# Performance work log

Hardware: AMD Instinct MI355X
Metric: run time of the kernel (lower is better)

Reference implementation:

```python
import jax, jax.numpy as jnp
import numpy as np


def setup_inputs() -> dict:
    key = jax.random.key(0)
    ks = jax.random.split(key, 8)
    B, E = 1024, 8
    dims = [480, 512, 512, 311]
    inp = {
        "x": jax.random.normal(ks[0], (B, dims[0]), dtype=jnp.float32),
        "weight_blend": jax.random.uniform(ks[1], (E, B), dtype=jnp.float32),
        "w0": jax.random.normal(ks[2], (E, dims[1], dims[0]), dtype=jnp.float32) * 0.05,
        "b0": jax.random.normal(ks[3], (E, dims[1]), dtype=jnp.float32) * 0.05,
        "w1": jax.random.normal(ks[4], (E, dims[2], dims[1]), dtype=jnp.float32) * 0.05,
        "b1": jax.random.normal(ks[5], (E, dims[2]), dtype=jnp.float32) * 0.05,
        "w2": jax.random.normal(ks[6], (E, dims[3], dims[2]), dtype=jnp.float32) * 0.05,
        "b2": jax.random.normal(ks[7], (E, dims[3]), dtype=jnp.float32) * 0.05,
    }
    return inp


def _blend_layer(h, blend, w, b):
    # Original: W_b = sum_e blend[e,b] * w[e]  (materializes [B, d_out, d_in]),
    # then matmul(W_b, h) + bias_b. Fused einsum computes identical math.
    out = jnp.einsum("eb,eoi,bi->bo", blend, w, h)
    out = out + jnp.einsum("eb,eo->bo", blend, b)
    return out


def reference(x, weight_blend, w0, b0, w1, b1, w2, b2):
    # dropout layers are identity (training=False / keep_prob=1)
    h = _blend_layer(x, weight_blend, w0, b0)
    h = jax.nn.elu(h)
    h = _blend_layer(h, weight_blend, w1, b1)
    h = jax.nn.elu(h)
    h = _blend_layer(h, weight_blend, w2, b2)  # no activation on final layer
    return h
```

## Files before the change

### kernel.cpp

```cpp
#include <hip/hip_runtime.h>

typedef __attribute__((ext_vector_type(8))) short short8;
typedef __attribute__((ext_vector_type(4))) float f32x4;

__device__ __forceinline__ unsigned short f2bf(float f) {
    unsigned u = __builtin_bit_cast(unsigned, f);
    unsigned r = (u + 0x7FFFu + ((u >> 16) & 1u)) >> 16;
    return (unsigned short)r;
}
__device__ __forceinline__ float bf2f(unsigned short u) {
    unsigned v = ((unsigned)u) << 16;
    return __builtin_bit_cast(float, v);
}

__device__ __forceinline__ void gload16(const unsigned short* g, unsigned short* l) {
    __builtin_amdgcn_global_load_lds(
        (const __attribute__((address_space(1))) void*)g,
        (__attribute__((address_space(3))) void*)l,
        16, 0, 0);
}

#define WAITV(N) asm volatile("s_waitcnt vmcnt(" #N ")" ::: "memory")
#define WAITL0() asm volatile("s_waitcnt lgkmcnt(0)" ::: "memory")
#define BAR() do { asm volatile("" ::: "memory"); __builtin_amdgcn_s_barrier(); asm volatile("" ::: "memory"); } while (0)

__device__ __forceinline__ short8 lds_read_swz(const unsigned short* tile, int row, int colb) {
    int off = row * 64 + colb;
    off ^= ((off >> 7) & 7) << 4;
    return *(const short8*)((const char*)tile + off);
}

__device__ __forceinline__ void cvt_chunk(const float* __restrict__ src,
                                          unsigned short* __restrict__ dst, int t) {
    const float4* s4 = (const float4*)src;
    float4 a = s4[2 * t], b = s4[2 * t + 1];
    union { unsigned short u[8]; int4 v; } r;
    r.u[0] = f2bf(a.x); r.u[1] = f2bf(a.y); r.u[2] = f2bf(a.z); r.u[3] = f2bf(a.w);
    r.u[4] = f2bf(b.x); r.u[5] = f2bf(b.y); r.u[6] = f2bf(b.z); r.u[7] = f2bf(b.w);
    ((int4*)dst)[t] = r.v;
}

__device__ __forceinline__ short8 pack8(float4 a, float4 b) {
    short8 p;
    p[0] = (short)f2bf(a.x); p[1] = (short)f2bf(a.y);
    p[2] = (short)f2bf(a.z); p[3] = (short)f2bf(a.w);
    p[4] = (short)f2bf(b.x); p[5] = (short)f2bf(b.y);
    p[6] = (short)f2bf(b.z); p[7] = (short)f2bf(b.w);
    return p;
}

__global__ __launch_bounds__(512) void k_gemm0(
    const float* __restrict__ A, const float* __restrict__ W,
    const float* __restrict__ blend, const float* __restrict__ bias,
    unsigned short* __restrict__ Y,
    const float* __restrict__ csrc, unsigned short* __restrict__ cdst)
{
    __shared__ unsigned short As[2][4096];
    __shared__ unsigned short Bs[2][4096];

    const int e  = blockIdx.z;
    const int bm = blockIdx.y * 128;
    const int on = blockIdx.x * 128;
    const int t  = threadIdx.x, lane = t & 63, w = t >> 6;
    const int wr = w >> 2, wc = w & 3;

    const int sr = lane >> 2, sce = (lane & 3) * 8;
    const int ra = w * 16 + sr;
    const float* gA = A + (size_t)(bm + ra) * 480 + sce;
    const float* gB = W + ((size_t)e * 512 + (on + ra)) * 480 + sce;

    int woff = ra * 64 + (lane & 3) * 16;
    woff ^= ((woff >> 7) & 7) << 4;

    float4 La0[3], La1[3], Lb0[3], Lb1[3];
    #pragma unroll
    for (int s = 0; s < 3; ++s) {
        int k0 = s * 32;
        La0[s] = *(const float4*)(gA + k0); La1[s] = *(const float4*)(gA + k0 + 4);
        Lb0[s] = *(const float4*)(gB + k0); Lb1[s] = *(const float4*)(gB + k0 + 4);
    }

    f32x4 acc[4][2] = {};

    #pragma unroll
    for (int kt = 0; kt < 15; ++kt) {
        const int s = kt % 3, buf = kt & 1;
        *(short8*)((char*)As[buf] + woff) = pack8(La0[s], La1[s]);
        *(short8*)((char*)Bs[buf] + woff) = pack8(Lb0[s], Lb1[s]);
        WAITL0();
        BAR();
        if (kt + 3 < 15) {
            int k0 = (kt + 3) * 32;
            La0[s] = *(const float4*)(gA + k0); La1[s] = *(const float4*)(gA + k0 + 4);
            Lb0[s] = *(const float4*)(gB + k0); Lb1[s] = *(const float4*)(gB + k0 + 4);
        }
        short8 af[4], bfr[2];
        #pragma unroll
        for (int fm = 0; fm < 4; ++fm)
            af[fm] = lds_read_swz(As[buf], wr * 64 + fm * 16 + (lane & 15), (lane >> 4) * 16);
        #pragma unroll
        for (int fn = 0; fn < 2; ++fn)
            bfr[fn] = lds_read_swz(Bs[buf], wc * 32 + fn * 16 + (lane & 15), (lane >> 4) * 16);
        #pragma unroll
        for (int fm = 0; fm < 4; ++fm)
            #pragma unroll
            for (int fn = 0; fn < 2; ++fn)
                acc[fm][fn] = __builtin_amdgcn_mfma_f32_16x16x32_bf16(
                    af[fm], bfr[fn], acc[fm][fn], 0, 0, 0);
    }

    const float* blendE = blend + e * 1024;
    const float* biasE  = bias + (size_t)e * 512;
    unsigned short* Ye  = Y + (size_t)e * 1024 * 512;
    #pragma unroll
    for (int fm = 0; fm < 4; ++fm) {
        int i0 = bm + wr * 64 + fm * 16 + (lane >> 4) * 4;
        float4 bl = *(const float4*)&blendE[i0];
        #pragma unroll
        for (int fn = 0; fn < 2; ++fn) {
            int j = on + wc * 32 + fn * 16 + (lane & 15);
            float bs = biasE[j];
            #pragma unroll
            for (int r = 0; r < 4; ++r)
                Ye[(size_t)(i0 + r) * 512 + j] = f2bf((acc[fm][fn][r] + bs) * ((&bl.x)[r]));
        }
    }

    int lb = (blockIdx.z * 8 + blockIdx.y) * 4 + blockIdx.x;
    cvt_chunk(csrc, cdst, lb * 1024 + threadIdx.x);
    cvt_chunk(csrc, cdst, lb * 1024 + 512 + threadIdx.x);
}

__global__ __launch_bounds__(512) void k_gemm(
    const unsigned short* __restrict__ A,
    const unsigned short* __restrict__ W,
    const float* __restrict__ blend, const float* __restrict__ bias,
    unsigned short* __restrict__ Y,
    int N, int ldy,
    const float* __restrict__ csrc, unsigned short* __restrict__ cdst, int nchunk)
{
    __shared__ unsigned short As[4][4096];
    __shared__ unsigned short Bs[4][4096];

    const int e  = blockIdx.z;
    const int bm = blockIdx.y * 128;
    const int on = blockIdx.x * 128;
    const int t  = threadIdx.x, lane = t & 63, w = t >> 6;
    const int wr = w >> 2, wc = w & 3;

    const unsigned short* Wt = W + (size_t)e * N * 512;
    const int l2 = lane ^ ((lane >> 3) & 7);
    const int sr = l2 >> 2, sce = (l2 & 3) * 8;
    const int ra = w * 16 + sr;
    int rb = on + ra; if (rb > N - 1) rb = N - 1;
    const unsigned short* gA = A  + (size_t)(bm + ra) * 512 + sce;
    const unsigned short* gB = Wt + (size_t)rb * 512 + sce;

#define STAGE(buf, kt) do { int _k0 = (kt) * 32;                       \
        gload16(gA + _k0, &As[(buf)][w * 512]);                        \
        gload16(gB + _k0, &Bs[(buf)][w * 512]); } while (0)

#define COMPUTE(cur) do {                                                          \
        short8 af[4], bfr[2];                                                      \
        _Pragma("unroll")                                                          \
        for (int fm = 0; fm < 4; ++fm)                                             \
            af[fm] = lds_read_swz(As[(cur)], wr * 64 + fm * 16 + (lane & 15), (lane >> 4) * 16); \
        _Pragma("unroll")                                                          \
        for (int fn = 0; fn < 2; ++fn)                                             \
            bfr[fn] = lds_read_swz(Bs[(cur)], wc * 32 + fn * 16 + (lane & 15), (lane >> 4) * 16); \
        _Pragma("unroll")                                                          \
        for (int fm = 0; fm < 4; ++fm)                                             \
            _Pragma("unroll")                                                      \
            for (int fn = 0; fn < 2; ++fn)                                         \
                acc[fm][fn] = __builtin_amdgcn_mfma_f32_16x16x32_bf16(             \
                    af[fm], bfr[fn], acc[fm][fn], 0, 0, 0);                        \
    } while (0)

    f32x4 acc[4][2] = {};
    STAGE(0, 0); STAGE(1, 1); STAGE(2, 2);

    for (int kt = 0; kt < 13; ++kt) {
        WAITV(4);
        BAR();
        STAGE((kt + 3) & 3, kt + 3);
        COMPUTE(kt & 3);
    }
    WAITV(4); BAR(); COMPUTE(1);
    WAITV(2); BAR(); COMPUTE(2);
    WAITV(0); BAR(); COMPUTE(3);
#undef STAGE

    const float* blendE = blend + e * 1024;
    const float* biasE  = bias + (size_t)e * N;
    unsigned short* Ye  = Y + (size_t)e * 1024 * ldy;
    #pragma unroll
    for (int fm = 0; fm < 4; ++fm) {
        int i0 = bm + wr * 64 + fm * 16 + (lane >> 4) * 4;
        float4 bl = *(const float4*)&blendE[i0];
        #pragma unroll
        for (int fn = 0; fn < 2; ++fn) {
            int j = on + wc * 32 + fn * 16 + (lane & 15);
            if (j < N) {
                float bs = biasE[j];
                #pragma unroll
                for (int r = 0; r < 4; ++r)
                    Ye[(size_t)(i0 + r) * ldy + j] = f2bf((acc[fm][fn][r] + bs) * ((&bl.x)[r]));
            }
        }
    }

    if (cdst) {
        int lb = (blockIdx.z * 8 + blockIdx.y) * gridDim.x + blockIdx.x;
        #pragma unroll
        for (int q = 0; q < 2; ++q) {
            int tl = q * 512 + threadIdx.x;
            if (tl < nchunk) cvt_chunk(csrc, cdst, lb * nchunk + tl);
        }
    }
}

__global__ __launch_bounds__(256) void k_reduce8(
    const unsigned short* __restrict__ Y, unsigned short* __restrict__ out)
{
    int idx = blockIdx.x * 256 + threadIdx.x;
    int b  = idx >> 6;
    int o0 = (idx & 63) * 8;
    size_t base = (size_t)b * 512 + o0;
    float s[8] = {};
    #pragma unroll
    for (int p = 0; p < 8; ++p) {
        int4 v = *(const int4*)&Y[base + (size_t)p * 1024 * 512];
        const unsigned short* u = (const unsigned short*)&v;
        #pragma unroll
        for (int r = 0; r < 8; ++r) s[r] += bf2f(u[r]);
    }
    union { unsigned short u[8]; int4 v; } rr;
    #pragma unroll
    for (int r = 0; r < 8; ++r) {
        float v = (s[r] > 0.f) ? s[r] : expm1f(s[r]);
        rr.u[r] = f2bf(v);
    }
    *(int4*)&out[base] = rr.v;
}

__global__ __launch_bounds__(256) void k_reduce_last(
    const unsigned short* __restrict__ Y, float* __restrict__ out)
{
    int idx = blockIdx.x * 256 + threadIdx.x;
    if (idx >= 1024 * 40) return;
    int b  = idx / 40;
    int o0 = (idx - b * 40) * 8;
    size_t base = (size_t)b * 320 + o0;
    float s[8] = {};
    #pragma unroll
    for (int p = 0; p < 8; ++p) {
        int4 v = *(const int4*)&Y[base + (size_t)p * 1024 * 320];
        const unsigned short* u = (const unsigned short*)&v;
        #pragma unroll
        for (int r = 0; r < 8; ++r) s[r] += bf2f(u[r]);
    }
    #pragma unroll
    for (int r = 0; r < 8; ++r)
        if (o0 + r < 311) out[(size_t)b * 311 + o0 + r] = s[r];
}

extern "C" void kernel_launch(void* const* d_in, const int* in_sizes, int n_in,
                              void* d_out, int out_size, void* d_ws, size_t ws_size,
                              hipStream_t stream) {
    const float* x     = (const float*)d_in[0];
    const float* blend = (const float*)d_in[1];
    const float* w0    = (const float*)d_in[2];
    const float* b0    = (const float*)d_in[3];
    const float* w1    = (const float*)d_in[4];
    const float* b1    = (const float*)d_in[5];
    const float* w2    = (const float*)d_in[6];
    const float* b2    = (const float*)d_in[7];

    char* ws = (char*)d_ws;
    unsigned short* w1b = (unsigned short*)(ws + 0);
    unsigned short* w2b = (unsigned short*)(ws + 4194304);
    unsigned short* h1b = (unsigned short*)(ws + 6742016);
    unsigned short* h2b = (unsigned short*)(ws + 7790592);
    unsigned short* yb  = (unsigned short*)(ws + 8839168);

    k_gemm0<<<dim3(4, 8, 8), 512, 0, stream>>>(x, w0, blend, b0, yb, w1, w1b);
    k_reduce8<<<256, 256, 0, stream>>>(yb, h1b);

    k_gemm<<<dim3(4, 8, 8), 512, 0, stream>>>(h1b, w1b, blend, b1, yb, 512, 512,
                                              w2, w2b, 622);
    k_reduce8<<<256, 256, 0, stream>>>(yb, h2b);

    k_gemm<<<dim3(3, 8, 8), 512, 0, stream>>>(h2b, w2b, blend, b2, yb, 311, 320,
                                              nullptr, nullptr, 0);
    k_reduce_last<<<160, 256, 0, stream>>>(yb, (float*)d_out);
}
```

Before: 54.13 us.

## Fuse expert-sum reduction and ELU into the next GEMM's A-tile load

Removes the two standalone reduce kernels and has each subsequent GEMM read all 8 per-expert partial outputs, sum them, and apply ELU while building the bf16 A tile in LDS. This saves two launches and the write and re-read of the reduced activations. In exchange, every GEMM block re-reads the 8 expert slices for its rows, so each reduction is repeated across all N-tiles and experts, which multiplies global traffic for A by 8 and adds ALU work. The async global_load_lds 4-stage pipeline is replaced by a register-staged double buffer.

```diff
diff --git a/kernel.cpp b/kernel.cpp
--- a/kernel.cpp
+++ b/kernel.cpp
@@ -11,13 +11,6 @@
 __device__ __forceinline__ float bf2f(unsigned short u) {
     unsigned v = ((unsigned)u) << 16;
     return __builtin_bit_cast(float, v);
-}
-
-__device__ __forceinline__ void gload16(const unsigned short* g, unsigned short* l) {
-    __builtin_amdgcn_global_load_lds(
-        (const __attribute__((address_space(1))) void*)g,
-        (__attribute__((address_space(3))) void*)l,
-        16, 0, 0);
 }
 
 #define WAITV(N) asm volatile("s_waitcnt vmcnt(" #N ")" ::: "memory")
@@ -48,117 +41,6 @@
     p[6] = (short)f2bf(b.z); p[7] = (short)f2bf(b.w);
     return p;
 }
-
-__global__ __launch_bounds__(512) void k_gemm0(
-    const float* __restrict__ A, const float* __restrict__ W,
-    const float* __restrict__ blend, const float* __restrict__ bias,
-    unsigned short* __restrict__ Y,
-    const float* __restrict__ csrc, unsigned short* __restrict__ cdst)
-{
-    __shared__ unsigned short As[2][4096];
-    __shared__ unsigned short Bs[2][4096];
-
-    const int e  = blockIdx.z;
-    const int bm = blockIdx.y * 128;
-    const int on = blockIdx.x * 128;
-    const int t  = threadIdx.x, lane = t & 63, w = t >> 6;
-    const int wr = w >> 2, wc = w & 3;
-
-    const int sr = lane >> 2, sce = (lane & 3) * 8;
-    const int ra = w * 16 + sr;
-    const float* gA = A + (size_t)(bm + ra) * 480 + sce;
-    const float* gB = W + ((size_t)e * 512 + (on + ra)) * 480 + sce;
-
-    int woff = ra * 64 + (lane & 3) * 16;
-    woff ^= ((woff >> 7) & 7) << 4;
-
-    float4 La0[3], La1[3], Lb0[3], Lb1[3];
-    #pragma unroll
-    for (int s = 0; s < 3; ++s) {
-        int k0 = s * 32;
-        La0[s] = *(const float4*)(gA + k0); La1[s] = *(const float4*)(gA + k0 + 4);
-        Lb0[s] = *(const float4*)(gB + k0); Lb1[s] = *(const float4*)(gB + k0 + 4);
-    }
-
-    f32x4 acc[4][2] = {};
-
-    #pragma unroll
-    for (int kt = 0; kt < 15; ++kt) {
-        const int s = kt % 3, buf = kt & 1;
-        *(short8*)((char*)As[buf] + woff) = pack8(La0[s], La1[s]);
-        *(short8*)((char*)Bs[buf] + woff) = pack8(Lb0[s], Lb1[s]);
-        WAITL0();
-        BAR();
-        if (kt + 3 < 15) {
-            int k0 = (kt + 3) * 32;
-            La0[s] = *(const float4*)(gA + k0); La1[s] = *(const float4*)(gA + k0 + 4);
-            Lb0[s] = *(const float4*)(gB + k0); Lb1[s] = *(const float4*)(gB + k0 + 4);
-        }
-        short8 af[4], bfr[2];
-        #pragma unroll
-        for (int fm = 0; fm < 4; ++fm)
-            af[fm] = lds_read_swz(As[buf], wr * 64 + fm * 16 + (lane & 15), (lane >> 4) * 16);
-        #pragma unroll
-        for (int fn = 0; fn < 2; ++fn)
-            bfr[fn] = lds_read_swz(Bs[buf], wc * 32 + fn * 16 + (lane & 15), (lane >> 4) * 16);
-        #pragma unroll
-        for (int fm = 0; fm < 4; ++fm)
-            #pragma unroll
-            for (int fn = 0; fn < 2; ++fn)
-                acc[fm][fn] = __builtin_amdgcn_mfma_f32_16x16x32_bf16(
-                    af[fm], bfr[fn], acc[fm][fn], 0, 0, 0);
-    }
-
-    const float* blendE = blend + e * 1024;
-    const float* biasE  = bias + (size_t)e * 512;
-    unsigned short* Ye  = Y + (size_t)e * 1024 * 512;
-    #pragma unroll
-    for (int fm = 0; fm < 4; ++fm) {
-        int i0 = bm + wr * 64 + fm * 16 + (lane >> 4) * 4;
-        float4 bl = *(const float4*)&blendE[i0];
-        #pragma unroll
-        for (int fn = 0; fn < 2; ++fn) {
-            int j = on + wc * 32 + fn * 16 + (lane & 15);
-            float bs = biasE[j];
-            #pragma unroll
-            for (int r = 0; r < 4; ++r)
-                Ye[(size_t)(i0 + r) * 512 + j] = f2bf((acc[fm][fn][r] + bs) * ((&bl.x)[r]));
-        }
-    }
-
-    int lb = (blockIdx.z * 8 + blockIdx.y) * 4 + blockIdx.x;
-    cvt_chunk(csrc, cdst, lb * 1024 + threadIdx.x);
-    cvt_chunk(csrc, cdst, lb * 1024 + 512 + threadIdx.x);
-}
-
-__global__ __launch_bounds__(512) void k_gemm(
-    const unsigned short* __restrict__ A,
-    const unsigned short* __restrict__ W,
-    const float* __restrict__ blend, const float* __restrict__ bias,
-    unsigned short* __restrict__ Y,
-    int N, int ldy,
-    const float* __restrict__ csrc, unsigned short* __restrict__ cdst, int nchunk)
-{
-    __shared__ unsigned short As[4][4096];
-    __shared__ unsigned short Bs[4][4096];
-
-    const int e  = blockIdx.z;
-    const int bm = blockIdx.y * 128;
-    const int on = blockIdx.x * 128;
-    const int t  = threadIdx.x, lane = t & 63, w = t >> 6;
-    const int wr = w >> 2, wc = w & 3;
-
-    const unsigned short* Wt = W + (size_t)e * N * 512;
-    const int l2 = lane ^ ((lane >> 3) & 7);
-    const int sr = l2 >> 2, sce = (l2 & 3) * 8;
-    const int ra = w * 16 + sr;
-    int rb = on + ra; if (rb > N - 1) rb = N - 1;
-    const unsigned short* gA = A  + (size_t)(bm + ra) * 512 + sce;
-    const unsigned short* gB = Wt + (size_t)rb * 512 + sce;
-
-#define STAGE(buf, kt) do { int _k0 = (kt) * 32;                       \
-        gload16(gA + _k0, &As[(buf)][w * 512]);                        \
-        gload16(gB + _k0, &Bs[(buf)][w * 512]); } while (0)
 
 #define COMPUTE(cur) do {                                                          \
         short8 af[4], bfr[2];                                                      \
@@ -176,23 +58,156 @@
                     af[fm], bfr[fn], acc[fm][fn], 0, 0, 0);                        \
     } while (0)
 
+__global__ __launch_bounds__(512) void k_gemm0(
+    const float* __restrict__ A, const float* __restrict__ W,
+    const float* __restrict__ blend, const float* __restrict__ bias,
+    unsigned short* __restrict__ Y,
+    const float* __restrict__ csrc, unsigned short* __restrict__ cdst)
+{
+    __shared__ unsigned short As[2][4096];
+    __shared__ unsigned short Bs[2][4096];
+
+    const int e  = blockIdx.z;
+    const int bm = blockIdx.y * 128;
+    const int on = blockIdx.x * 128;
+    const int t  = threadIdx.x, lane = t & 63, w = t >> 6;
+    const int wr = w >> 2, wc = w & 3;
+
+    const int sr = lane >> 2, sce = (lane & 3) * 8;
+    const int ra = w * 16 + sr;
+    const float* gA = A + (size_t)(bm + ra) * 480 + sce;
+    const float* gB = W + ((size_t)e * 512 + (on + ra)) * 480 + sce;
+
+    int woff = ra * 64 + (lane & 3) * 16;
+    woff ^= ((woff >> 7) & 7) << 4;
+
+    float4 La0[3], La1[3], Lb0[3], Lb1[3];
+    #pragma unroll
+    for (int s = 0; s < 3; ++s) {
+        int k0 = s * 32;
+        La0[s] = *(const float4*)(gA + k0); La1[s] = *(const float4*)(gA + k0 + 4);
+        Lb0[s] = *(const float4*)(gB + k0); Lb1[s] = *(const float4*)(gB + k0 + 4);
+    }
+
     f32x4 acc[4][2] = {};
-    STAGE(0, 0); STAGE(1, 1); STAGE(2, 2);
-
-    for (int kt = 0; kt < 13; ++kt) {
-        WAITV(4);
+
+    #pragma unroll
+    for (int kt = 0; kt < 15; ++kt) {
+        const int s = kt % 3, buf = kt & 1;
+        *(short8*)((char*)As[buf] + woff) = pack8(La0[s], La1[s]);
+        *(short8*)((char*)Bs[buf] + woff) = pack8(Lb0[s], Lb1[s]);
+        WAITL0();
         BAR();
-        STAGE((kt + 3) & 3, kt + 3);
-        COMPUTE(kt & 3);
-    }
-    WAITV(4); BAR(); COMPUTE(1);
-    WAITV(2); BAR(); COMPUTE(2);
-    WAITV(0); BAR(); COMPUTE(3);
-#undef STAGE
+        if (kt + 3 < 15) {
+            int k0 = (kt + 3) * 32;
+            La0[s] = *(const float4*)(gA + k0); La1[s] = *(const float4*)(gA + k0 + 4);
+            Lb0[s] = *(const float4*)(gB + k0); Lb1[s] = *(const float4*)(gB + k0 + 4);
+        }
+        COMPUTE(buf);
+    }
+
+    const float* blendE = blend + e * 1024;
+    const float* biasE  = bias + (size_t)e * 512;
+    unsigned short* Ye  = Y + (size_t)e * 1024 * 512;
+    #pragma unroll
+    for (int fm = 0; fm < 4; ++fm) {
+        int i0 = bm + wr * 64 + fm * 16 + (lane >> 4) * 4;
+        float4 bl = *(const float4*)&blendE[i0];
+        #pragma unroll
+        for (int fn = 0; fn < 2; ++fn) {
+            int j = on + wc * 32 + fn * 16 + (lane & 15);
+            float bs = biasE[j];
+            #pragma unroll
+            for (int r = 0; r < 4; ++r)
+                Ye[(size_t)(i0 + r) * 512 + j] = f2bf((acc[fm][fn][r] + bs) * ((&bl.x)[r]));
+        }
+    }
+
+    int lb = (blockIdx.z * 8 + blockIdx.y) * 4 + blockIdx.x;
+    cvt_chunk(csrc, cdst, lb * 1024 + threadIdx.x);
+    cvt_chunk(csrc, cdst, lb * 1024 + 512 + threadIdx.x);
+}
+
+__global__ __launch_bounds__(512) void k_gemm_rho(
+    const unsigned short* __restrict__ Yin,
+    const unsigned short* __restrict__ W,
+    const float* __restrict__ blend, const float* __restrict__ bias,
+    unsigned short* __restrict__ Yout,
+    int N, int ldy,
+    const float* __restrict__ csrc, unsigned short* __restrict__ cdst, int nchunk)
+{
+    __shared__ unsigned short As[2][4096];
+    __shared__ unsigned short Bs[2][4096];
+
+    const int e  = blockIdx.z;
+    const int bm = blockIdx.y * 128;
+    const int on = blockIdx.x * 128;
+    const int t  = threadIdx.x, lane = t & 63, w = t >> 6;
+    const int wr = w >> 2, wc = w & 3;
+
+    const int sr = lane >> 2, sc8 = (lane & 3) * 8;
+    const int ra = w * 16 + sr;
+    const unsigned short* gA = Yin + (size_t)(bm + ra) * 512 + sc8;
+    int rb = on + ra; if (rb > N - 1) rb = N - 1;
+    const unsigned short* gB = W + ((size_t)e * N + rb) * 512 + sc8;
+
+    int woff = ra * 64 + (lane & 3) * 16;
+    woff ^= ((woff >> 7) & 7) << 4;
+
+    int4 Ar0[8], Ar1[8], Br0, Br1;
+    #pragma unroll
+    for (int p = 0; p < 8; ++p) Ar0[p] = *(const int4*)(gA + (size_t)p * 524288);
+    Br0 = *(const int4*)(gB);
+    #pragma unroll
+    for (int p = 0; p < 8; ++p) Ar1[p] = *(const int4*)(gA + (size_t)p * 524288 + 32);
+    Br1 = *(const int4*)(gB + 32);
+
+    f32x4 acc[4][2] = {};
+
+    #pragma unroll
+    for (int kt = 0; kt < 16; ++kt) {
+        const int s = kt & 1;
+        if (kt == 15) { WAITV(0); } else { WAITV(9); }
+
+        float h[8];
+        #pragma unroll
+        for (int j = 0; j < 8; ++j) h[j] = 0.f;
+        #pragma unroll
+        for (int p = 0; p < 8; ++p) {
+            const unsigned short* u = s ? (const unsigned short*)&Ar1[p]
+                                        : (const unsigned short*)&Ar0[p];
+            #pragma unroll
+            for (int j = 0; j < 8; ++j) h[j] += bf2f(u[j]);
+        }
+        short8 aw;
+        #pragma unroll
+        for (int j = 0; j < 8; ++j) {
+            float v = (h[j] > 0.f) ? h[j] : (__expf(h[j]) - 1.0f);
+            aw[j] = (short)f2bf(v);
+        }
+        *(short8*)((char*)As[s] + woff) = aw;
+        *(short8*)((char*)Bs[s] + woff) = s ? *(const short8*)&Br1 : *(const short8*)&Br0;
+        WAITL0();
+        BAR();
+
+        if (kt + 2 < 16) {
+            int c = (kt + 2) * 32;
+            if (s) {
+                #pragma unroll
+                for (int p = 0; p < 8; ++p) Ar1[p] = *(const int4*)(gA + (size_t)p * 524288 + c);
+                Br1 = *(const int4*)(gB + c);
+            } else {
+                #pragma unroll
+                for (int p = 0; p < 8; ++p) Ar0[p] = *(const int4*)(gA + (size_t)p * 524288 + c);
+                Br0 = *(const int4*)(gB + c);
+            }
+        }
+        COMPUTE(s);
+    }
 
     const float* blendE = blend + e * 1024;
     const float* biasE  = bias + (size_t)e * N;
-    unsigned short* Ye  = Y + (size_t)e * 1024 * ldy;
+    unsigned short* Ye  = Yout + (size_t)e * 1024 * ldy;
     #pragma unroll
     for (int fm = 0; fm < 4; ++fm) {
         int i0 = bm + wr * 64 + fm * 16 + (lane >> 4) * 4;
@@ -217,30 +232,6 @@
             if (tl < nchunk) cvt_chunk(csrc, cdst, lb * nchunk + tl);
         }
     }
-}
-
-__global__ __launch_bounds__(256) void k_reduce8(
-    const unsigned short* __restrict__ Y, unsigned short* __restrict__ out)
-{
-    int idx = blockIdx.x * 256 + threadIdx.x;
-    int b  = idx >> 6;
-    int o0 = (idx & 63) * 8;
-    size_t base = (size_t)b * 512 + o0;
-    float s[8] = {};
-    #pragma unroll
-    for (int p = 0; p < 8; ++p) {
-        int4 v = *(const int4*)&Y[base + (size_t)p * 1024 * 512];
-        const unsigned short* u = (const unsigned short*)&v;
-        #pragma unroll
-        for (int r = 0; r < 8; ++r) s[r] += bf2f(u[r]);
-    }
-    union { unsigned short u[8]; int4 v; } rr;
-    #pragma unroll
-    for (int r = 0; r < 8; ++r) {
-        float v = (s[r] > 0.f) ? s[r] : expm1f(s[r]);
-        rr.u[r] = f2bf(v);
-    }
-    *(int4*)&out[base] = rr.v;
 }
 
 __global__ __launch_bounds__(256) void k_reduce_last(
@@ -279,18 +270,16 @@
     char* ws = (char*)d_ws;
     unsigned short* w1b = (unsigned short*)(ws + 0);
     unsigned short* w2b = (unsigned short*)(ws + 4194304);
-    unsigned short* h1b = (unsigned short*)(ws + 6742016);
-    unsigned short* h2b = (unsigned short*)(ws + 7790592);
-    unsigned short* yb  = (unsigned short*)(ws + 8839168);
+    unsigned short* yb  = (unsigned short*)(ws + 6742016);
+    unsigned short* yb2 = (unsigned short*)(ws + 15130624);
 
     k_gemm0<<<dim3(4, 8, 8), 512, 0, stream>>>(x, w0, blend, b0, yb, w1, w1b);
-    k_reduce8<<<256, 256, 0, stream>>>(yb, h1b);
-
-    k_gemm<<<dim3(4, 8, 8), 512, 0, stream>>>(h1b, w1b, blend, b1, yb, 512, 512,
-                                              w2, w2b, 622);
-    k_reduce8<<<256, 256, 0, stream>>>(yb, h2b);
-
-    k_gemm<<<dim3(3, 8, 8), 512, 0, stream>>>(h2b, w2b, blend, b2, yb, 311, 320,
-                                              nullptr, nullptr, 0);
+
+    k_gemm_rho<<<dim3(4, 8, 8), 512, 0, stream>>>(yb, w1b, blend, b1, yb2, 512, 512,
+                                                  w2, w2b, 622);
+
+    k_gemm_rho<<<dim3(3, 8, 8), 512, 0, stream>>>(yb2, w2b, blend, b2, yb, 311, 320,
+                                                  nullptr, nullptr, 0);
+
     k_reduce_last<<<160, 256, 0, stream>>>(yb, (float*)d_out);
 }
```

New measurement: 75.13 us. 1.39x slower.

## Use 64-wide K tiles with double buffering in GEMM kernel

Applied to the files above, without the earlier changes.

Changes the k_gemm main loop from a 4-stage pipeline of 32-wide K tiles to a 2-stage double buffer of 64-wide K tiles, with 8 iterations instead of 16. Each stage now issues four direct-to-LDS loads per thread and runs two MFMA sub-steps. A new swizzle function handles the 128-byte row stride. The goal is to halve barrier and waitcnt overhead per K. The cost is a shallower prefetch depth, since each iteration waits for all loads (vmcnt 0), which may expose more memory latency.

```diff
diff --git a/kernel.cpp b/kernel.cpp
--- a/kernel.cpp
+++ b/kernel.cpp
@@ -24,8 +24,13 @@
 #define WAITL0() asm volatile("s_waitcnt lgkmcnt(0)" ::: "memory")
 #define BAR() do { asm volatile("" ::: "memory"); __builtin_amdgcn_s_barrier(); asm volatile("" ::: "memory"); } while (0)
 
-__device__ __forceinline__ short8 lds_read_swz(const unsigned short* tile, int row, int colb) {
+__device__ __forceinline__ short8 lds_read_swz32(const unsigned short* tile, int row, int colb) {
     int off = row * 64 + colb;
+    off ^= ((off >> 7) & 7) << 4;
+    return *(const short8*)((const char*)tile + off);
+}
+__device__ __forceinline__ short8 lds_read_swz64(const unsigned short* tile, int row, int colb) {
+    int off = row * 128 + colb;
     off ^= ((off >> 7) & 7) << 4;
     return *(const short8*)((const char*)tile + off);
 }
@@ -97,10 +102,10 @@
         short8 af[4], bfr[2];
         #pragma unroll
         for (int fm = 0; fm < 4; ++fm)
-            af[fm] = lds_read_swz(As[buf], wr * 64 + fm * 16 + (lane & 15), (lane >> 4) * 16);
+            af[fm] = lds_read_swz32(As[buf], wr * 64 + fm * 16 + (lane & 15), (lane >> 4) * 16);
         #pragma unroll
         for (int fn = 0; fn < 2; ++fn)
-            bfr[fn] = lds_read_swz(Bs[buf], wc * 32 + fn * 16 + (lane & 15), (lane >> 4) * 16);
+            bfr[fn] = lds_read_swz32(Bs[buf], wc * 32 + fn * 16 + (lane & 15), (lane >> 4) * 16);
         #pragma unroll
         for (int fm = 0; fm < 4; ++fm)
             #pragma unroll
@@ -139,8 +144,8 @@
     int N, int ldy,
     const float* __restrict__ csrc, unsigned short* __restrict__ cdst, int nchunk)
 {
-    __shared__ unsigned short As[4][4096];
-    __shared__ unsigned short Bs[4][4096];
+    __shared__ unsigned short As[2][8192];
+    __shared__ unsigned short Bs[2][8192];
 
     const int e  = blockIdx.z;
     const int bm = blockIdx.y * 128;
@@ -149,45 +154,49 @@
     const int wr = w >> 2, wc = w & 3;
 
     const unsigned short* Wt = W + (size_t)e * N * 512;
-    const int l2 = lane ^ ((lane >> 3) & 7);
-    const int sr = l2 >> 2, sce = (l2 & 3) * 8;
-    const int ra = w * 16 + sr;
-    int rb = on + ra; if (rb > N - 1) rb = N - 1;
-    const unsigned short* gA = A  + (size_t)(bm + ra) * 512 + sce;
-    const unsigned short* gB = Wt + (size_t)rb * 512 + sce;
-
-#define STAGE(buf, kt) do { int _k0 = (kt) * 32;                       \
-        gload16(gA + _k0, &As[(buf)][w * 512]);                        \
-        gload16(gB + _k0, &Bs[(buf)][w * 512]); } while (0)
-
-#define COMPUTE(cur) do {                                                          \
-        short8 af[4], bfr[2];                                                      \
-        _Pragma("unroll")                                                          \
-        for (int fm = 0; fm < 4; ++fm)                                             \
-            af[fm] = lds_read_swz(As[(cur)], wr * 64 + fm * 16 + (lane & 15), (lane >> 4) * 16); \
-        _Pragma("unroll")                                                          \
-        for (int fn = 0; fn < 2; ++fn)                                             \
-            bfr[fn] = lds_read_swz(Bs[(cur)], wc * 32 + fn * 16 + (lane & 15), (lane >> 4) * 16); \
-        _Pragma("unroll")                                                          \
-        for (int fm = 0; fm < 4; ++fm)                                             \
-            _Pragma("unroll")                                                      \
-            for (int fn = 0; fn < 2; ++fn)                                         \
-                acc[fm][fn] = __builtin_amdgcn_mfma_f32_16x16x32_bf16(             \
-                    af[fm], bfr[fn], acc[fm][fn], 0, 0, 0);                        \
-    } while (0)
+    const int srow = w * 8 + (lane >> 3);
+    const int scol = 8 * ((lane & 7) ^ ((lane >> 3) & 7));
+    const unsigned short* gA0 = A + (size_t)(bm + srow) * 512 + scol;
+    const unsigned short* gA1 = A + (size_t)(bm + 64 + srow) * 512 + scol;
+    int rb0 = on + srow;      if (rb0 > N - 1) rb0 = N - 1;
+    int rb1 = on + 64 + srow; if (rb1 > N - 1) rb1 = N - 1;
+    const unsigned short* gB0 = Wt + (size_t)rb0 * 512 + scol;
+    const unsigned short* gB1 = Wt + (size_t)rb1 * 512 + scol;
+
+#define STAGE(buf, kt) do { int _k = (kt) * 64;                        \
+        gload16(gA0 + _k, &As[(buf)][t * 8]);                          \
+        gload16(gA1 + _k, &As[(buf)][4096 + t * 8]);                   \
+        gload16(gB0 + _k, &Bs[(buf)][t * 8]);                          \
+        gload16(gB1 + _k, &Bs[(buf)][4096 + t * 8]); } while (0)
 
     f32x4 acc[4][2] = {};
-    STAGE(0, 0); STAGE(1, 1); STAGE(2, 2);
-
-    for (int kt = 0; kt < 13; ++kt) {
-        WAITV(4);
+    STAGE(0, 0);
+
+    #pragma unroll
+    for (int kt = 0; kt < 8; ++kt) {
+        const int cur = kt & 1;
+        WAITV(0);
         BAR();
-        STAGE((kt + 3) & 3, kt + 3);
-        COMPUTE(kt & 3);
-    }
-    WAITV(4); BAR(); COMPUTE(1);
-    WAITV(2); BAR(); COMPUTE(2);
-    WAITV(0); BAR(); COMPUTE(3);
+        if (kt + 1 < 8) STAGE(cur ^ 1, kt + 1);
+        #pragma unroll
+        for (int ks = 0; ks < 2; ++ks) {
+            short8 af[4], bfr[2];
+            #pragma unroll
+            for (int fm = 0; fm < 4; ++fm)
+                af[fm] = lds_read_swz64(As[cur], wr * 64 + fm * 16 + (lane & 15),
+                                        ks * 64 + (lane >> 4) * 16);
+            #pragma unroll
+            for (int fn = 0; fn < 2; ++fn)
+                bfr[fn] = lds_read_swz64(Bs[cur], wc * 32 + fn * 16 + (lane & 15),
+                                         ks * 64 + (lane >> 4) * 16);
+            #pragma unroll
+            for (int fm = 0; fm < 4; ++fm)
+                #pragma unroll
+                for (int fn = 0; fn < 2; ++fn)
+                    acc[fm][fn] = __builtin_amdgcn_mfma_f32_16x16x32_bf16(
+                        af[fm], bfr[fn], acc[fm][fn], 0, 0, 0);
+        }
+    }
 #undef STAGE
 
     const float* blendE = blend + e * 1024;
```

After: 55.54 us. 2.6% more time.
